# Kernel tuning notes

Hardware: AMD Instinct MI355X
Metric: run time of the kernel (lower is better)

The kernel has to match this reference:

```python
import jax, jax.numpy as jnp
import numpy as np
from jax import lax

B, C_IN, H, W = 128, 3, 32, 32
HC, HHC, P, NCLS = 32, 128, 4, 10
STEPS_PER_PIECE = 1           # fixed-step RK4: 1 step per unit-length piece
DT = 1.0 / STEPS_PER_PIECE
DIMNUMS = ('NCHW', 'OIHW', 'NCHW')


def setup_inputs() -> dict:
    key = jax.random.key(0)
    ks = jax.random.split(key, 8)
    def rn(k, shape, fan_in):
        return jax.random.normal(k, shape, jnp.float32) / np.sqrt(fan_in).astype(np.float32)
    return {
        'x': jax.random.normal(ks[0], (B, C_IN, H, W), jnp.float32),
        'y': jax.random.randint(ks[1], (B,), 0, NCLS),
        'aug_W': rn(ks[2], (HC, C_IN), C_IN),
        'aug_b': jnp.zeros((HC,), jnp.float32),
        'W1': rn(ks[3], (P, HHC, 1 + HC), 1 + HC),      # stacked 1x1 conv weights per piece
        'b1': jnp.zeros((P, HHC), jnp.float32),
        'W2': rn(ks[4], (P, HHC, HHC, 3, 3), HHC * 9),  # stacked 3x3 conv weights per piece
        'b2': jnp.zeros((P, HHC), jnp.float32),
        'W3': rn(ks[5], (P, HC, HHC), HHC),             # stacked 1x1 conv weights per piece
        'b3': jnp.zeros((P, HC), jnp.float32),
        'ro_W': rn(ks[6], (NCLS, HC * H * W), HC * H * W),
        'ro_b': jnp.zeros((NCLS,), jnp.float32),
    }


def _func(t, z, W1, b1, W2, b2, W3, b3):
    # piece selection: bisect(range(P+1), t) - 1, clipped -> floor(t) clipped to [0, P-1]
    idx = jnp.clip(jnp.floor(t).astype(jnp.int32), 0, P - 1)
    w1, v1 = W1[idx], b1[idx]
    w2, v2 = W2[idx], b2[idx]
    w3, v3 = W3[idx], b3[idx]
    # broadcast time as an extra channel and concat: [B, 1+HC, H, W]
    tc = jnp.full((z.shape[0], 1, z.shape[2], z.shape[3]), t, z.dtype)
    h = jnp.concatenate([tc, z], axis=1)
    h = jax.nn.softplus(jnp.einsum('bchw,oc->bohw', h, w1) + v1[:, None, None])
    h = lax.conv_general_dilated(h, w2, (1, 1), 'SAME', dimension_numbers=DIMNUMS)
    h = jax.nn.softplus(h + v2[None, :, None, None])
    h = jnp.einsum('bchw,oc->bohw', h, w3) + v3[:, None, None]
    return jnp.tanh(h)  # tanh=True


def reference(x, y, aug_W, aug_b, W1, b1, W2, b2, W3, b3, ro_W, ro_b):
    # augment: Linear over channel dim (transpose(1,3) trick == 1x1 conv)
    z = jnp.einsum('bchw,oc->bohw', x, aug_W) + aug_b[:, None, None]

    def f(t, zz):
        return _func(t, zz, W1, b1, W2, b2, W3, b3)

    dt = jnp.float32(DT)
    t0s = jnp.arange(P * STEPS_PER_PIECE, dtype=jnp.float32) * dt

    def rk4_step(zz, t0):
        k1 = f(t0, zz)
        k2 = f(t0 + dt / 2, zz + (dt / 2) * k1)
        k3 = f(t0 + dt / 2, zz + (dt / 2) * k2)
        k4 = f(t0 + dt, zz + dt * k3)
        return zz + (dt / 6) * (k1 + 2 * k2 + 2 * k3 + k4), None

    zT, _ = lax.scan(rk4_step, z, t0s)

    logits = zT.reshape(zT.shape[0], -1) @ ro_W.T + ro_b
    logp = jax.nn.log_softmax(logits, axis=-1)
    loss = -jnp.mean(jnp.take_along_axis(logp, y[:, None], axis=1))
    accuracy = (jnp.argmax(logits, axis=1) == y).sum().astype(logits.dtype)
    return loss, accuracy
```

## Files before the change

kernel.cpp:

```cpp
#include <hip/hip_runtime.h>
#include <hip/hip_bf16.h>
#include <math.h>

#define BN   128
#define CIN  3
#define HCn  32
#define HHCn 128
#define NPX  1024
#define PN   4
#define NCLS 10

#define PLROW 8
#define PLSZ  1664
#define H2P   136

#define PGPU  9728
#define IMGU  77824

typedef short bf16x8 __attribute__((ext_vector_type(8)));
typedef float f32x4  __attribute__((ext_vector_type(4)));

__device__ __forceinline__ float softplus_f(float x) {
    return fmaxf(x, 0.f) + __logf(1.f + __expf(-fabsf(x)));
}
__device__ __forceinline__ float tanh_fast(float x) {
    float e = __expf(-2.f * fabsf(x));
    float r = 1.f - 2.f * e * __builtin_amdgcn_rcpf(1.f + e);
    unsigned u = (__float_as_uint(r) & 0x7fffffffu) | (__float_as_uint(x) & 0x80000000u);
    return __uint_as_float(u);
}
__device__ __forceinline__ unsigned int f2bf(float f) {
    unsigned int u = __float_as_uint(f);
    return (u + 0x7fffu + ((u >> 16) & 1u)) >> 16;
}
__device__ __forceinline__ float bf2f(unsigned int h) {
    return __uint_as_float(h << 16);
}
__device__ __forceinline__ void pack2(float a, float b, unsigned int& hi, unsigned int& lo) {
    __hip_bfloat162 h2 = __float22bfloat162_rn(float2{a, b});
    unsigned int h = *reinterpret_cast<unsigned int*>(&h2);
    float ha = __uint_as_float(h << 16);
    float hb = __uint_as_float(h & 0xffff0000u);
    __hip_bfloat162 l2 = __float22bfloat162_rn(float2{a - ha, b - hb});
    hi = h;
    lo = *reinterpret_cast<unsigned int*>(&l2);
}

__global__ __launch_bounds__(256) void k_aug(
    const float* __restrict__ x, const float* __restrict__ aW,
    const float* __restrict__ ab, float* __restrict__ z,
    unsigned short* __restrict__ pz0)
{
    const int b = blockIdx.x, tid = threadIdx.x;
    const size_t xb = (size_t)b * CIN * NPX;
    const size_t zb = (size_t)b * HCn * NPX;
    unsigned short* pzi = pz0 + (size_t)b * IMGU;
    float xv[CIN][4];
#pragma unroll
    for (int c = 0; c < CIN; c++)
#pragma unroll
        for (int j = 0; j < 4; j++)
            xv[c][j] = x[xb + c * NPX + tid + 256 * j];
#pragma unroll
    for (int plane = 0; plane < 4; plane++) {
        float v[8][4];
#pragma unroll
        for (int s = 0; s < 8; s++) {
            int o = plane * 8 + s;
            float w0 = aW[o * 3], w1 = aW[o * 3 + 1], w2 = aW[o * 3 + 2], bb = ab[o];
#pragma unroll
            for (int j = 0; j < 4; j++) {
                float vv = fmaf(w0, xv[0][j], fmaf(w1, xv[1][j], fmaf(w2, xv[2][j], bb)));
                v[s][j] = vv;
                z[zb + (size_t)o * NPX + tid + 256 * j] = vv;
            }
        }
#pragma unroll
        for (int j = 0; j < 4; j++) {
            int pix = tid + 256 * j;
            int row = ((pix >> 5) + 1) * 34 + (pix & 31) + 1;
            unsigned int h01, l01, h23, l23, h45, l45, h67, l67;
            pack2(v[0][j], v[1][j], h01, l01);
            pack2(v[2][j], v[3][j], h23, l23);
            pack2(v[4][j], v[5][j], h45, l45);
            pack2(v[6][j], v[7][j], h67, l67);
            *(uint4*)(pzi + (size_t)plane * PGPU + row * 8) = make_uint4(h01, h23, h45, h67);
            *(uint4*)(pzi + (size_t)(4 + plane) * PGPU + row * 8) = make_uint4(l01, l23, l45, l67);
        }
    }
}

__global__ __launch_bounds__(256) void k_packW2(
    const float* __restrict__ W2, unsigned short* __restrict__ whi,
    unsigned short* __restrict__ wlo)
{
    int t = blockIdx.x * 256 + threadIdx.x;
    int j    = t & 7;
    int lane = (t >> 3) & 63;
    int ocg  = (t >> 9) & 7;
    int kc   = (t >> 12) & 3;
    int p9s  = t >> 14;
    int sh = p9s % 9, p = p9s / 9;
    int dy = sh / 3, dx = sh % 3;
    int oc = ocg * 16 + (lane & 15);
    int ic = kc * 32 + (lane >> 4) * 8 + j;
    float v = W2[((((size_t)p * HHCn + oc) * HHCn + ic) * 3 + dy) * 3 + dx];
    unsigned int hi = f2bf(v);
    whi[t] = (unsigned short)hi;
    wlo[t] = (unsigned short)f2bf(v - bf2f(hi));
}

__global__ __launch_bounds__(256) void k_packW1(
    const float* __restrict__ W1, unsigned short* __restrict__ whi,
    unsigned short* __restrict__ wlo)
{
    int t = blockIdx.x * 256 + threadIdx.x;
    int j = t & 7, lane = (t >> 3) & 63, m = (t >> 9) & 1, kc = (t >> 10) & 3, p = t >> 12;
    int oc = kc * 32 + m * 16 + (lane & 15);
    int ic = (lane >> 4) * 8 + j;
    float v = W1[((size_t)p * HHCn + oc) * 33 + 1 + ic];
    unsigned int hi = f2bf(v);
    whi[t] = (unsigned short)hi;
    wlo[t] = (unsigned short)f2bf(v - bf2f(hi));
}

__global__ __launch_bounds__(256) void k_packW3(
    const float* __restrict__ W3, unsigned short* __restrict__ whi,
    unsigned short* __restrict__ wlo)
{
    int t = blockIdx.x * 256 + threadIdx.x;
    int j = t & 7, lane = (t >> 3) & 63, kk = (t >> 9) & 3, m = (t >> 11) & 1, p = t >> 12;
    int st = m * 16 + (lane & 15);
    int ic = kk * 32 + (lane >> 4) * 8 + j;
    float v = W3[((size_t)p * HCn + st) * HHCn + ic];
    unsigned int hi = f2bf(v);
    whi[t] = (unsigned short)hi;
    wlo[t] = (unsigned short)f2bf(v - bf2f(hi));
}

__global__ __launch_bounds__(512, 4) void k_fused(
    const float* __restrict__ z_in, const unsigned short* __restrict__ pz_in,
    const float* __restrict__ b1p, const float* __restrict__ W1t, float t,
    const unsigned short* __restrict__ w1h, const unsigned short* __restrict__ w1l,
    const unsigned short* __restrict__ w2h, const unsigned short* __restrict__ w2l,
    const float* __restrict__ b2p,
    const unsigned short* __restrict__ w3h, const unsigned short* __restrict__ w3l,
    const float* __restrict__ b3p,
    float* __restrict__ accb, float* __restrict__ z_out,
    unsigned short* __restrict__ pz_out, float alpha_next, int mode)
{
    const int strip = blockIdx.x, b = blockIdx.y;
    const int tid = threadIdx.x, lane = tid & 63, wid = tid >> 6;
    const int ln15 = lane & 15, lg = lane >> 4;
    const int kl8 = lg * 8, kl4 = lg * 4;

    __shared__ __align__(16) unsigned short S[39936];
    unsigned short* zinh = S;
    unsigned short* zinl = S + 6656;
    unsigned short* xh0  = S + 13312;
    unsigned short* xl0  = S + 19968;
    unsigned short* xh1  = S + 26624;
    unsigned short* xl1  = S + 33280;
    unsigned short* h2qh = S;
    unsigned short* h2ql = S + 8704;

    {
        const unsigned short* src0 = pz_in + (size_t)b * IMGU;
        const int rowoff = strip * 136;
#pragma unroll
        for (int i = 0; i < 4; i++) {
            int c = tid + 512 * i;
            if (c < 1664) {
                int region = c / 208;
                int row = c - region * 208;
                uint4 d = *(const uint4*)(src0 + (size_t)region * PGPU + (size_t)(rowoff + row) * 8);
                *(uint4*)(S + region * 1664 + row * 8) = d;
            }
        }
    }

    const int wocg = (wid & 3) * 2;
    const int wph  = (wid >> 2) * 64;
    const int strip0 = strip * 4;
    int boff[4];
#pragma unroll
    for (int f = 0; f < 4; f++) {
        int pxl = wph + f * 16 + ln15;
        boff[f] = lg * PLSZ + ((pxl >> 5) * 34 + (pxl & 31)) * PLROW;
    }

    f32x4 acc[2][4];
#pragma unroll
    for (int o = 0; o < 2; o++)
#pragma unroll
        for (int f = 0; f < 4; f++) acc[o][f] = (f32x4)(0.f);

    f32x4 c1[2][2];

    auto do_conv1 = [&](int kc) {
        const unsigned short* w1hb = w1h + (size_t)kc * 1024 + lane * 8;
        const unsigned short* w1lb = w1l + (size_t)kc * 1024 + lane * 8;
        bf16x8 a1h0 = *(const bf16x8*)w1hb, a1h1 = *(const bf16x8*)(w1hb + 512);
        bf16x8 a1l0 = *(const bf16x8*)w1lb, a1l1 = *(const bf16x8*)(w1lb + 512);
#pragma unroll
        for (int m = 0; m < 2; m++)
#pragma unroll
            for (int ni = 0; ni < 2; ni++) c1[m][ni] = (f32x4)(0.f);
        __builtin_amdgcn_s_setprio(1);
#pragma unroll
        for (int ni = 0; ni < 2; ni++) {
            int n = wid + 8 * ni;
            if (ni == 0 || wid < 5) {
                int roff = lg * PLSZ + (n * 16 + ln15) * PLROW;
                bf16x8 bh = *(const bf16x8*)(zinh + roff);
                bf16x8 bl = *(const bf16x8*)(zinl + roff);
                c1[0][ni] = __builtin_amdgcn_mfma_f32_16x16x32_bf16(a1h0, bh, c1[0][ni], 0, 0, 0);
                c1[0][ni] = __builtin_amdgcn_mfma_f32_16x16x32_bf16(a1h0, bl, c1[0][ni], 0, 0, 0);
                c1[0][ni] = __builtin_amdgcn_mfma_f32_16x16x32_bf16(a1l0, bh, c1[0][ni], 0, 0, 0);
                c1[1][ni] = __builtin_amdgcn_mfma_f32_16x16x32_bf16(a1h1, bh, c1[1][ni], 0, 0, 0);
                c1[1][ni] = __builtin_amdgcn_mfma_f32_16x16x32_bf16(a1h1, bl, c1[1][ni], 0, 0, 0);
                c1[1][ni] = __builtin_amdgcn_mfma_f32_16x16x32_bf16(a1l1, bh, c1[1][ni], 0, 0, 0);
            }
        }
        __builtin_amdgcn_s_setprio(0);
    };

    auto do_writeX = [&](int kc, unsigned short* xh_, unsigned short* xl_) {
        float eb[2][4];
#pragma unroll
        for (int m = 0; m < 2; m++)
#pragma unroll
            for (int r = 0; r < 4; r++) {
                int oc = kc * 32 + m * 16 + kl4 + r;
                eb[m][r] = b1p[oc] + t * W1t[oc * 33];
            }
#pragma unroll
        for (int ni = 0; ni < 2; ni++) {
            int n = wid + 8 * ni;
            if (ni == 0 || wid < 5) {
                int ppad = n * 16 + ln15;
                int prow = ppad / 34, pcol = ppad - prow * 34;
                int gy = strip0 + prow - 1;
                bool zero = (pcol == 0) || (pcol == 33) || (gy < 0) || (gy >= 32);
#pragma unroll
                for (int m = 0; m < 2; m++) {
                    float v[4];
#pragma unroll
                    for (int r = 0; r < 4; r++)
                        v[r] = zero ? 0.f : softplus_f(c1[m][ni][r] + eb[m][r]);
                    unsigned int h01, l01, h23, l23;
                    pack2(v[0], v[1], h01, l01);
                    pack2(v[2], v[3], h23, l23);
                    int off = (m * 2 + (kl4 >> 3)) * PLSZ + ppad * PLROW + (kl4 & 7);
                    *(uint2*)(xh_ + off) = make_uint2(h01, h23);
                    *(uint2*)(xl_ + off) = make_uint2(l01, l23);
                }
            }
        }
    };

    auto do_conv3 = [&](int kc, const unsigned short* xh_, const unsigned short* xl_) {
        __builtin_amdgcn_s_setprio(1);
#pragma unroll
        for (int sh = 0; sh < 9; sh++) {
            const size_t wbase = ((size_t)(sh * 4 + kc) * 8 + wocg) * 512 + lane * 8;
            bf16x8 ah0 = *(const bf16x8*)(w2h + wbase);
            bf16x8 al0 = *(const bf16x8*)(w2l + wbase);
            bf16x8 ah1 = *(const bf16x8*)(w2h + wbase + 512);
            bf16x8 al1 = *(const bf16x8*)(w2l + wbase + 512);
            const int soff = ((sh / 3) * 34 + (sh % 3)) * PLROW;
#pragma unroll
            for (int f = 0; f < 4; f++) {
                bf16x8 bh = *(const bf16x8*)(xh_ + boff[f] + soff);
                bf16x8 bl = *(const bf16x8*)(xl_ + boff[f] + soff);
                acc[0][f] = __builtin_amdgcn_mfma_f32_16x16x32_bf16(ah0, bh, acc[0][f], 0, 0, 0);
                acc[0][f] = __builtin_amdgcn_mfma_f32_16x16x32_bf16(ah0, bl, acc[0][f], 0, 0, 0);
                acc[0][f] = __builtin_amdgcn_mfma_f32_16x16x32_bf16(al0, bh, acc[0][f], 0, 0, 0);
                acc[1][f] = __builtin_amdgcn_mfma_f32_16x16x32_bf16(ah1, bh, acc[1][f], 0, 0, 0);
                acc[1][f] = __builtin_amdgcn_mfma_f32_16x16x32_bf16(ah1, bl, acc[1][f], 0, 0, 0);
                acc[1][f] = __builtin_amdgcn_mfma_f32_16x16x32_bf16(al1, bh, acc[1][f], 0, 0, 0);
            }
        }
        __builtin_amdgcn_s_setprio(0);
    };

    __syncthreads();
    do_conv1(0);
    do_writeX(0, xh0, xl0);
    __syncthreads();

    do_conv1(1); do_writeX(1, xh1, xl1); do_conv3(0, xh0, xl0);
    __syncthreads();
    do_conv1(2); do_writeX(2, xh0, xl0); do_conv3(1, xh1, xl1);
    __syncthreads();
    do_conv1(3); do_writeX(3, xh1, xl1); do_conv3(2, xh0, xl0);
    __syncthreads();
    do_conv3(3, xh1, xl1);

    float bb2[2][4];
#pragma unroll
    for (int o2 = 0; o2 < 2; o2++)
#pragma unroll
        for (int r = 0; r < 4; r++)
            bb2[o2][r] = b2p[(wocg + o2) * 16 + kl4 + r];

    const size_t obB = (size_t)b * HCn * NPX + strip * 128;
    const int m3 = wid & 1, n4 = wid >> 1;
    float bb3[4];
#pragma unroll
    for (int r = 0; r < 4; r++) bb3[r] = b3p[m3 * 16 + kl4 + r];

#pragma unroll
    for (int q = 0; q < 2; q++) {
        __syncthreads();
        if ((wid >> 2) == q) {
#pragma unroll
            for (int o2 = 0; o2 < 2; o2++)
#pragma unroll
                for (int f2 = 0; f2 < 4; f2++) {
                    f32x4 a = acc[o2][f2];
                    float v[4];
#pragma unroll
                    for (int r = 0; r < 4; r++) v[r] = softplus_f(a[r] + bb2[o2][r]);
                    unsigned int h01, l01, h23, l23;
                    pack2(v[0], v[1], h01, l01);
                    pack2(v[2], v[3], h23, l23);
                    int off = (f2 * 16 + ln15) * H2P + (wocg + o2) * 16 + kl4;
                    *(uint2*)(h2qh + off) = make_uint2(h01, h23);
                    *(uint2*)(h2ql + off) = make_uint2(l01, l23);
                }
        }
        __syncthreads();
        f32x4 c3 = (f32x4)(0.f);
        __builtin_amdgcn_s_setprio(1);
#pragma unroll
        for (int kk = 0; kk < 4; kk++) {
            const unsigned short* a3hb = w3h + (size_t)(m3 * 4 + kk) * 512 + lane * 8;
            const unsigned short* a3lb = w3l + (size_t)(m3 * 4 + kk) * 512 + lane * 8;
            bf16x8 a3h = *(const bf16x8*)a3hb;
            bf16x8 a3l = *(const bf16x8*)a3lb;
            bf16x8 bh = *(const bf16x8*)(h2qh + (n4 * 16 + ln15) * H2P + kk * 32 + kl8);
            bf16x8 bl = *(const bf16x8*)(h2ql + (n4 * 16 + ln15) * H2P + kk * 32 + kl8);
            c3 = __builtin_amdgcn_mfma_f32_16x16x32_bf16(a3h, bh, c3, 0, 0, 0);
            c3 = __builtin_amdgcn_mfma_f32_16x16x32_bf16(a3h, bl, c3, 0, 0, 0);
            c3 = __builtin_amdgcn_mfma_f32_16x16x32_bf16(a3l, bh, c3, 0, 0, 0);
        }
        __builtin_amdgcn_s_setprio(0);
        const int st0 = m3 * 16 + kl4;
        const int pix = strip * 128 + q * 64 + n4 * 16 + ln15;
        const int prow_g = ((pix >> 5) + 1) * 34 + (pix & 31) + 1;
        float pk[4];
#pragma unroll
        for (int r = 0; r < 4; r++) {
            int st = st0 + r;
            float v = tanh_fast(c3[r] + bb3[r]);
            size_t i = obB + (size_t)st * NPX + q * 64 + n4 * 16 + ln15;
            float zv = z_in[i];
            if (mode == 0)      { accb[i] = v;           pk[r] = fmaf(alpha_next, v, zv); }
            else if (mode == 1) { accb[i] += 2.f * v;    pk[r] = fmaf(alpha_next, v, zv); }
            else { float zn = zv + (accb[i] + v) * (1.f / 6.f); z_out[i] = zn; pk[r] = zn; }
        }
        unsigned int h01, l01, h23, l23;
        pack2(pk[0], pk[1], h01, l01);
        pack2(pk[2], pk[3], h23, l23);
        unsigned short* dsth = pz_out + (size_t)b * IMGU + (size_t)(st0 >> 3) * PGPU
                               + (size_t)prow_g * 8 + (st0 & 7);
        *(uint2*)dsth = make_uint2(h01, h23);
        *(uint2*)(dsth + (size_t)4 * PGPU) = make_uint2(l01, l23);
    }
}

__global__ __launch_bounds__(256) void k_logits(
    const float* __restrict__ z, const float* __restrict__ roW,
    const float* __restrict__ rob, float* __restrict__ logits)
{
    const int b = blockIdx.x, tid = threadIdx.x;
    float p[NCLS];
#pragma unroll
    for (int c = 0; c < NCLS; c++) p[c] = 0.f;
    const float* zp = z + (size_t)b * 32768;
    for (int i = tid; i < 32768; i += 256) {
        float zv = zp[i];
#pragma unroll
        for (int c = 0; c < NCLS; c++) p[c] = fmaf(zv, roW[(size_t)c * 32768 + i], p[c]);
    }
#pragma unroll
    for (int c = 0; c < NCLS; c++)
        for (int off = 32; off > 0; off >>= 1) p[c] += __shfl_down(p[c], off, 64);
    __shared__ float red[4][NCLS];
    int wid = tid >> 6, lane = tid & 63;
    if (lane == 0)
#pragma unroll
        for (int c = 0; c < NCLS; c++) red[wid][c] = p[c];
    __syncthreads();
    if (tid < NCLS) {
        float s = red[0][tid] + red[1][tid] + red[2][tid] + red[3][tid] + rob[tid];
        logits[b * NCLS + tid] = s;
    }
}

__global__ __launch_bounds__(128) void k_loss(
    const float* __restrict__ logits, const int* __restrict__ y,
    float* __restrict__ out)
{
    const int b = threadIdx.x;
    float l[NCLS];
#pragma unroll
    for (int c = 0; c < NCLS; c++) l[c] = logits[b * NCLS + c];
    float m = l[0]; int am = 0;
#pragma unroll
    for (int c = 1; c < NCLS; c++) if (l[c] > m) { m = l[c]; am = c; }
    float s = 0.f;
#pragma unroll
    for (int c = 0; c < NCLS; c++) s += expf(l[c] - m);
    float lse = m + logf(s);
    int yy = y[b];
    float loss_b = lse - l[yy];
    float corr = (am == yy) ? 1.f : 0.f;
    for (int off = 32; off > 0; off >>= 1) {
        loss_b += __shfl_down(loss_b, off, 64);
        corr   += __shfl_down(corr,   off, 64);
    }
    __shared__ float sl[2], sc[2];
    if ((b & 63) == 0) { sl[b >> 6] = loss_b; sc[b >> 6] = corr; }
    __syncthreads();
    if (b == 0) {
        out[0] = (sl[0] + sl[1]) / (float)BN;
        out[1] = sc[0] + sc[1];
    }
}

extern "C" void kernel_launch(void* const* d_in, const int* in_sizes, int n_in,
                              void* d_out, int out_size, void* d_ws, size_t ws_size,
                              hipStream_t stream) {
    const float* x   = (const float*)d_in[0];
    const int*   y   = (const int*)  d_in[1];
    const float* aW  = (const float*)d_in[2];
    const float* ab  = (const float*)d_in[3];
    const float* W1  = (const float*)d_in[4];
    const float* b1  = (const float*)d_in[5];
    const float* W2  = (const float*)d_in[6];
    const float* b2  = (const float*)d_in[7];
    const float* W3  = (const float*)d_in[8];
    const float* b3  = (const float*)d_in[9];
    const float* roW = (const float*)d_in[10];
    const float* rob = (const float*)d_in[11];
    float* out = (float*)d_out;
    float* ws  = (float*)d_ws;

    const size_t ZSZ = (size_t)BN * HCn * NPX;
    float* zb0    = ws;
    float* zb1    = zb0 + ZSZ;
    float* accb   = zb1 + ZSZ;
    float* logits = accb + ZSZ;
    unsigned short* w2h = (unsigned short*)(logits + 4096);
    unsigned short* w2l = w2h + 589824;
    unsigned short* w1h = w2l + 589824;
    unsigned short* w1l = w1h + 16384;
    unsigned short* w3h = w1l + 16384;
    unsigned short* w3l = w3h + 16384;
    unsigned short* pz0 = w3l + 16384;
    unsigned short* pz1 = pz0 + (size_t)BN * IMGU;

    hipMemsetAsync(pz0, 0, (size_t)2 * BN * IMGU * sizeof(unsigned short), stream);

    k_packW2<<<2304, 256, 0, stream>>>(W2, w2h, w2l);
    k_packW1<<<64, 256, 0, stream>>>(W1, w1h, w1l);
    k_packW3<<<64, 256, 0, stream>>>(W3, w3h, w3l);
    k_aug<<<BN, 256, 0, stream>>>(x, aW, ab, zb0, pz0);

    float* zA = zb0;
    float* zB = zb1;
    unsigned short* pza = pz0;
    unsigned short* pzb = pz1;
    for (int ge = 0; ge < 16; ge++) {
        const int p = ge >> 2, e = ge & 3;
        const int idx = (e == 3 && p + 1 < PN) ? p + 1 : p;
        const float t = (float)p + (e == 0 ? 0.f : (e == 3 ? 1.f : 0.5f));
        const int mode = (e == 0) ? 0 : (e == 3 ? 2 : 1);
        const float alpha_next = (e == 2) ? 1.f : ((e == 3) ? 0.f : 0.5f);
        k_fused<<<dim3(8, BN), 512, 0, stream>>>(
            zA, pza,
            b1 + (size_t)idx * HHCn, W1 + (size_t)idx * HHCn * 33, t,
            w1h + (size_t)idx * 4096, w1l + (size_t)idx * 4096,
            w2h + (size_t)idx * 147456, w2l + (size_t)idx * 147456,
            b2 + (size_t)idx * HHCn,
            w3h + (size_t)idx * 4096, w3l + (size_t)idx * 4096,
            b3 + (size_t)idx * HCn,
            accb, zB, pzb, alpha_next, mode);
        unsigned short* tp = pza; pza = pzb; pzb = tp;
        if (e == 3) { float* tz = zA; zA = zB; zB = tz; }
    }

    k_logits<<<BN, 256, 0, stream>>>(zA, roW, rob, logits);
    k_loss<<<1, 128, 0, stream>>>(logits, y, out);
}
```

Before: 1.970 ms.

## Warp-specialize fused ODE kernel into conv1 producer and conv3x3 consumer waves

Splits the 8 waves into 4 producer waves that compute the 1x1 conv plus softplus into shared staging buffers, and 4 consumer waves that run the 3x3 conv MFMAs over a 64-channel by 64-pixel tile each. Previously every wave did both stages in lockstep. The hidden activation for the final 1x1 conv is now written to shared memory in one pass instead of two half passes, which drops two barriers. The trade-off is that consumer waves hold twice as many accumulators, raising register pressure, and only half the waves issue the dominant 3x3 MFMA work, so total throughput may drop.

```diff
diff --git a/kernel.cpp b/kernel.cpp
--- a/kernel.cpp
+++ b/kernel.cpp
@@ -161,8 +161,8 @@
     unsigned short* xl0  = S + 19968;
     unsigned short* xh1  = S + 26624;
     unsigned short* xl1  = S + 33280;
-    unsigned short* h2qh = S;
-    unsigned short* h2ql = S + 8704;
+    unsigned short* h2h  = S;
+    unsigned short* h2l  = S + 17408;
 
     {
         const unsigned short* src0 = pz_in + (size_t)b * IMGU;
@@ -179,53 +179,49 @@
         }
     }
 
-    const int wocg = (wid & 3) * 2;
-    const int wph  = (wid >> 2) * 64;
+    const bool isP = (wid < 4);
+    const int pw = wid & 3;
+    const int och = pw & 1;
+    const int pxh = pw >> 1;
     const int strip0 = strip * 4;
+
     int boff[4];
 #pragma unroll
     for (int f = 0; f < 4; f++) {
-        int pxl = wph + f * 16 + ln15;
+        int pxl = pxh * 64 + f * 16 + ln15;
         boff[f] = lg * PLSZ + ((pxl >> 5) * 34 + (pxl & 31)) * PLROW;
     }
 
-    f32x4 acc[2][4];
-#pragma unroll
-    for (int o = 0; o < 2; o++)
-#pragma unroll
-        for (int f = 0; f < 4; f++) acc[o][f] = (f32x4)(0.f);
-
-    f32x4 c1[2][2];
-
-    auto do_conv1 = [&](int kc) {
+    f32x4 acc[4][4];
+    f32x4 c1[4][2];
+
+    auto conv1P = [&](int kc) {
         const unsigned short* w1hb = w1h + (size_t)kc * 1024 + lane * 8;
         const unsigned short* w1lb = w1l + (size_t)kc * 1024 + lane * 8;
         bf16x8 a1h0 = *(const bf16x8*)w1hb, a1h1 = *(const bf16x8*)(w1hb + 512);
         bf16x8 a1l0 = *(const bf16x8*)w1lb, a1l1 = *(const bf16x8*)(w1lb + 512);
 #pragma unroll
-        for (int m = 0; m < 2; m++)
-#pragma unroll
-            for (int ni = 0; ni < 2; ni++) c1[m][ni] = (f32x4)(0.f);
-        __builtin_amdgcn_s_setprio(1);
-#pragma unroll
-        for (int ni = 0; ni < 2; ni++) {
-            int n = wid + 8 * ni;
-            if (ni == 0 || wid < 5) {
+        for (int ni = 0; ni < 4; ni++)
+#pragma unroll
+            for (int m = 0; m < 2; m++) c1[ni][m] = (f32x4)(0.f);
+#pragma unroll
+        for (int ni = 0; ni < 4; ni++) {
+            int n = pw + 4 * ni;
+            if (n < 13) {
                 int roff = lg * PLSZ + (n * 16 + ln15) * PLROW;
                 bf16x8 bh = *(const bf16x8*)(zinh + roff);
                 bf16x8 bl = *(const bf16x8*)(zinl + roff);
-                c1[0][ni] = __builtin_amdgcn_mfma_f32_16x16x32_bf16(a1h0, bh, c1[0][ni], 0, 0, 0);
-                c1[0][ni] = __builtin_amdgcn_mfma_f32_16x16x32_bf16(a1h0, bl, c1[0][ni], 0, 0, 0);
-                c1[0][ni] = __builtin_amdgcn_mfma_f32_16x16x32_bf16(a1l0, bh, c1[0][ni], 0, 0, 0);
-                c1[1][ni] = __builtin_amdgcn_mfma_f32_16x16x32_bf16(a1h1, bh, c1[1][ni], 0, 0, 0);
-                c1[1][ni] = __builtin_amdgcn_mfma_f32_16x16x32_bf16(a1h1, bl, c1[1][ni], 0, 0, 0);
-                c1[1][ni] = __builtin_amdgcn_mfma_f32_16x16x32_bf16(a1l1, bh, c1[1][ni], 0, 0, 0);
-            }
-        }
-        __builtin_amdgcn_s_setprio(0);
+                c1[ni][0] = __builtin_amdgcn_mfma_f32_16x16x32_bf16(a1h0, bh, c1[ni][0], 0, 0, 0);
+                c1[ni][0] = __builtin_amdgcn_mfma_f32_16x16x32_bf16(a1h0, bl, c1[ni][0], 0, 0, 0);
+                c1[ni][0] = __builtin_amdgcn_mfma_f32_16x16x32_bf16(a1l0, bh, c1[ni][0], 0, 0, 0);
+                c1[ni][1] = __builtin_amdgcn_mfma_f32_16x16x32_bf16(a1h1, bh, c1[ni][1], 0, 0, 0);
+                c1[ni][1] = __builtin_amdgcn_mfma_f32_16x16x32_bf16(a1h1, bl, c1[ni][1], 0, 0, 0);
+                c1[ni][1] = __builtin_amdgcn_mfma_f32_16x16x32_bf16(a1l1, bh, c1[ni][1], 0, 0, 0);
+            }
+        }
     };
 
-    auto do_writeX = [&](int kc, unsigned short* xh_, unsigned short* xl_) {
+    auto writeXP = [&](int kc, unsigned short* xh_, unsigned short* xl_) {
         float eb[2][4];
 #pragma unroll
         for (int m = 0; m < 2; m++)
@@ -235,9 +231,9 @@
                 eb[m][r] = b1p[oc] + t * W1t[oc * 33];
             }
 #pragma unroll
-        for (int ni = 0; ni < 2; ni++) {
-            int n = wid + 8 * ni;
-            if (ni == 0 || wid < 5) {
+        for (int ni = 0; ni < 4; ni++) {
+            int n = pw + 4 * ni;
+            if (n < 13) {
                 int ppad = n * 16 + ln15;
                 int prow = ppad / 34, pcol = ppad - prow * 34;
                 int gy = strip0 + prow - 1;
@@ -247,7 +243,7 @@
                     float v[4];
 #pragma unroll
                     for (int r = 0; r < 4; r++)
-                        v[r] = zero ? 0.f : softplus_f(c1[m][ni][r] + eb[m][r]);
+                        v[r] = zero ? 0.f : softplus_f(c1[ni][m][r] + eb[m][r]);
                     unsigned int h01, l01, h23, l23;
                     pack2(v[0], v[1], h01, l01);
                     pack2(v[2], v[3], h23, l23);
@@ -259,78 +255,88 @@
         }
     };
 
-    auto do_conv3 = [&](int kc, const unsigned short* xh_, const unsigned short* xl_) {
+    auto conv3C = [&](int kc, const unsigned short* xh_, const unsigned short* xl_) {
         __builtin_amdgcn_s_setprio(1);
 #pragma unroll
         for (int sh = 0; sh < 9; sh++) {
-            const size_t wbase = ((size_t)(sh * 4 + kc) * 8 + wocg) * 512 + lane * 8;
-            bf16x8 ah0 = *(const bf16x8*)(w2h + wbase);
-            bf16x8 al0 = *(const bf16x8*)(w2l + wbase);
-            bf16x8 ah1 = *(const bf16x8*)(w2h + wbase + 512);
-            bf16x8 al1 = *(const bf16x8*)(w2l + wbase + 512);
             const int soff = ((sh / 3) * 34 + (sh % 3)) * PLROW;
 #pragma unroll
-            for (int f = 0; f < 4; f++) {
-                bf16x8 bh = *(const bf16x8*)(xh_ + boff[f] + soff);
-                bf16x8 bl = *(const bf16x8*)(xl_ + boff[f] + soff);
-                acc[0][f] = __builtin_amdgcn_mfma_f32_16x16x32_bf16(ah0, bh, acc[0][f], 0, 0, 0);
-                acc[0][f] = __builtin_amdgcn_mfma_f32_16x16x32_bf16(ah0, bl, acc[0][f], 0, 0, 0);
-                acc[0][f] = __builtin_amdgcn_mfma_f32_16x16x32_bf16(al0, bh, acc[0][f], 0, 0, 0);
-                acc[1][f] = __builtin_amdgcn_mfma_f32_16x16x32_bf16(ah1, bh, acc[1][f], 0, 0, 0);
-                acc[1][f] = __builtin_amdgcn_mfma_f32_16x16x32_bf16(ah1, bl, acc[1][f], 0, 0, 0);
-                acc[1][f] = __builtin_amdgcn_mfma_f32_16x16x32_bf16(al1, bh, acc[1][f], 0, 0, 0);
+            for (int op = 0; op < 2; op++) {
+                const size_t wbase = ((size_t)(sh * 4 + kc) * 8 + och * 4 + op * 2) * 512 + lane * 8;
+                bf16x8 ah0 = *(const bf16x8*)(w2h + wbase);
+                bf16x8 al0 = *(const bf16x8*)(w2l + wbase);
+                bf16x8 ah1 = *(const bf16x8*)(w2h + wbase + 512);
+                bf16x8 al1 = *(const bf16x8*)(w2l + wbase + 512);
+#pragma unroll
+                for (int f = 0; f < 4; f++) {
+                    bf16x8 bh = *(const bf16x8*)(xh_ + boff[f] + soff);
+                    bf16x8 bl = *(const bf16x8*)(xl_ + boff[f] + soff);
+                    acc[op * 2][f]     = __builtin_amdgcn_mfma_f32_16x16x32_bf16(ah0, bh, acc[op * 2][f], 0, 0, 0);
+                    acc[op * 2 + 1][f] = __builtin_amdgcn_mfma_f32_16x16x32_bf16(ah1, bh, acc[op * 2 + 1][f], 0, 0, 0);
+                    acc[op * 2][f]     = __builtin_amdgcn_mfma_f32_16x16x32_bf16(ah0, bl, acc[op * 2][f], 0, 0, 0);
+                    acc[op * 2 + 1][f] = __builtin_amdgcn_mfma_f32_16x16x32_bf16(ah1, bl, acc[op * 2 + 1][f], 0, 0, 0);
+                    acc[op * 2][f]     = __builtin_amdgcn_mfma_f32_16x16x32_bf16(al0, bh, acc[op * 2][f], 0, 0, 0);
+                    acc[op * 2 + 1][f] = __builtin_amdgcn_mfma_f32_16x16x32_bf16(al1, bh, acc[op * 2 + 1][f], 0, 0, 0);
+                }
             }
         }
         __builtin_amdgcn_s_setprio(0);
     };
 
     __syncthreads();
-    do_conv1(0);
-    do_writeX(0, xh0, xl0);
-    __syncthreads();
-
-    do_conv1(1); do_writeX(1, xh1, xl1); do_conv3(0, xh0, xl0);
-    __syncthreads();
-    do_conv1(2); do_writeX(2, xh0, xl0); do_conv3(1, xh1, xl1);
-    __syncthreads();
-    do_conv1(3); do_writeX(3, xh1, xl1); do_conv3(2, xh0, xl0);
-    __syncthreads();
-    do_conv3(3, xh1, xl1);
-
-    float bb2[2][4];
-#pragma unroll
-    for (int o2 = 0; o2 < 2; o2++)
-#pragma unroll
-        for (int r = 0; r < 4; r++)
-            bb2[o2][r] = b2p[(wocg + o2) * 16 + kl4 + r];
+    if (isP) { conv1P(0); writeXP(0, xh0, xl0); }
+    else {
+#pragma unroll
+        for (int o = 0; o < 4; o++)
+#pragma unroll
+            for (int f = 0; f < 4; f++) acc[o][f] = (f32x4)(0.f);
+    }
+    __syncthreads();
+
+    if (isP) { conv1P(1); writeXP(1, xh1, xl1); } else conv3C(0, xh0, xl0);
+    __syncthreads();
+    if (isP) { conv1P(2); writeXP(2, xh0, xl0); } else conv3C(1, xh1, xl1);
+    __syncthreads();
+    if (isP) { conv1P(3); writeXP(3, xh1, xl1); } else conv3C(2, xh0, xl0);
+    __syncthreads();
+    if (!isP) conv3C(3, xh1, xl1);
+    __syncthreads();
+
+    if (!isP) {
+        float bb2[4][4];
+#pragma unroll
+        for (int o = 0; o < 4; o++)
+#pragma unroll
+            for (int r = 0; r < 4; r++)
+                bb2[o][r] = b2p[och * 64 + o * 16 + kl4 + r];
+#pragma unroll
+        for (int o = 0; o < 4; o++)
+#pragma unroll
+            for (int f = 0; f < 4; f++) {
+                f32x4 a = acc[o][f];
+                float v[4];
+#pragma unroll
+                for (int r = 0; r < 4; r++) v[r] = softplus_f(a[r] + bb2[o][r]);
+                unsigned int h01, l01, h23, l23;
+                pack2(v[0], v[1], h01, l01);
+                pack2(v[2], v[3], h23, l23);
+                int px = pxh * 64 + f * 16 + ln15;
+                int off = px * H2P + och * 64 + o * 16 + kl4;
+                *(uint2*)(h2h + off) = make_uint2(h01, h23);
+                *(uint2*)(h2l + off) = make_uint2(l01, l23);
+            }
+    }
+    __syncthreads();
 
     const size_t obB = (size_t)b * HCn * NPX + strip * 128;
-    const int m3 = wid & 1, n4 = wid >> 1;
+    const int m3 = wid & 1, n8 = wid >> 1;
     float bb3[4];
 #pragma unroll
     for (int r = 0; r < 4; r++) bb3[r] = b3p[m3 * 16 + kl4 + r];
 
 #pragma unroll
-    for (int q = 0; q < 2; q++) {
-        __syncthreads();
-        if ((wid >> 2) == q) {
-#pragma unroll
-            for (int o2 = 0; o2 < 2; o2++)
-#pragma unroll
-                for (int f2 = 0; f2 < 4; f2++) {
-                    f32x4 a = acc[o2][f2];
-                    float v[4];
-#pragma unroll
-                    for (int r = 0; r < 4; r++) v[r] = softplus_f(a[r] + bb2[o2][r]);
-                    unsigned int h01, l01, h23, l23;
-                    pack2(v[0], v[1], h01, l01);
-                    pack2(v[2], v[3], h23, l23);
-                    int off = (f2 * 16 + ln15) * H2P + (wocg + o2) * 16 + kl4;
-                    *(uint2*)(h2qh + off) = make_uint2(h01, h23);
-                    *(uint2*)(h2ql + off) = make_uint2(l01, l23);
-                }
-        }
-        __syncthreads();
+    for (int jt = 0; jt < 2; jt++) {
+        const int nt = n8 * 2 + jt;
         f32x4 c3 = (f32x4)(0.f);
         __builtin_amdgcn_s_setprio(1);
 #pragma unroll
@@ -339,22 +345,22 @@
             const unsigned short* a3lb = w3l + (size_t)(m3 * 4 + kk) * 512 + lane * 8;
             bf16x8 a3h = *(const bf16x8*)a3hb;
             bf16x8 a3l = *(const bf16x8*)a3lb;
-            bf16x8 bh = *(const bf16x8*)(h2qh + (n4 * 16 + ln15) * H2P + kk * 32 + kl8);
-            bf16x8 bl = *(const bf16x8*)(h2ql + (n4 * 16 + ln15) * H2P + kk * 32 + kl8);
+            bf16x8 bh = *(const bf16x8*)(h2h + (nt * 16 + ln15) * H2P + kk * 32 + kl8);
+            bf16x8 bl = *(const bf16x8*)(h2l + (nt * 16 + ln15) * H2P + kk * 32 + kl8);
             c3 = __builtin_amdgcn_mfma_f32_16x16x32_bf16(a3h, bh, c3, 0, 0, 0);
             c3 = __builtin_amdgcn_mfma_f32_16x16x32_bf16(a3h, bl, c3, 0, 0, 0);
             c3 = __builtin_amdgcn_mfma_f32_16x16x32_bf16(a3l, bh, c3, 0, 0, 0);
         }
         __builtin_amdgcn_s_setprio(0);
         const int st0 = m3 * 16 + kl4;
-        const int pix = strip * 128 + q * 64 + n4 * 16 + ln15;
+        const int pix = strip * 128 + nt * 16 + ln15;
         const int prow_g = ((pix >> 5) + 1) * 34 + (pix & 31) + 1;
         float pk[4];
 #pragma unroll
         for (int r = 0; r < 4; r++) {
             int st = st0 + r;
             float v = tanh_fast(c3[r] + bb3[r]);
-            size_t i = obB + (size_t)st * NPX + q * 64 + n4 * 16 + ln15;
+            size_t i = obB + (size_t)st * NPX + nt * 16 + ln15;
             float zv = z_in[i];
             if (mode == 0)      { accb[i] = v;           pk[r] = fmaf(alpha_next, v, zv); }
             else if (mode == 1) { accb[i] += 2.f * v;    pk[r] = fmaf(alpha_next, v, zv); }
```

Result: slower. 2.321 ms (+17.8%).
